# Optimization experiments

Hardware: AMD Instinct MI355X
Metric: run time of the kernel (lower is better)

Reference implementation:

```python
import jax, jax.numpy as jnp
import numpy as np

B, N, C = 16, 8192, 64
NPOINT, NSAMPLE = 1024, 32
RADIUS = 0.1


def setup_inputs() -> dict:
    key = jax.random.key(0)
    ks = jax.random.split(key, 6)
    xyz = jax.random.uniform(ks[0], (B, N, 3), jnp.float32)          # points in unit cube
    features = jax.random.normal(ks[1], (B, C, N), jnp.float32)
    W1 = jax.random.normal(ks[2], (64, 67), jnp.float32) * 0.1
    b1 = jnp.zeros((64,), jnp.float32)
    W2 = jax.random.normal(ks[3], (64, 64), jnp.float32) * 0.1
    b2 = jnp.zeros((64,), jnp.float32)
    W3 = jax.random.normal(ks[4], (128, 64), jnp.float32) * 0.1
    b3 = jnp.zeros((128,), jnp.float32)
    return dict(xyz=xyz, features=features, W1=W1, b1=b1, W2=W2, b2=b2, W3=W3, b3=b3)


def _fps(pts, npoint):
    """Furthest point sampling on a single cloud pts:(N,3) -> (npoint,) int32 indices."""
    n = pts.shape[0]
    def step(carry, _):
        dist, far = carry
        d = jnp.sum((pts - pts[far]) ** 2, axis=-1)   # (N,)
        dist = jnp.minimum(dist, d)
        return (dist, jnp.argmax(dist).astype(jnp.int32)), far
    init = (jnp.full((n,), 1e10, pts.dtype), jnp.int32(0))
    _, idx = jax.lax.scan(step, init, None, length=npoint)
    return idx


def reference(xyz, features, W1, b1, W2, b2, W3, b3):
    n = xyz.shape[1]
    # --- furthest point sample + gather centroids ---
    idx = jax.lax.stop_gradient(jax.vmap(lambda p: _fps(p, NPOINT))(xyz))   # (B,npoint)
    new_xyz = jnp.take_along_axis(xyz, idx[:, :, None], axis=1)             # (B,npoint,3)
    # --- ball query: first NSAMPLE indices with dist < r, pad with first hit (0 if none) ---
    d2 = jnp.sum((new_xyz[:, :, None, :] - xyz[:, None, :, :]) ** 2, axis=-1)  # (B,npoint,N)
    cand = jnp.where(d2 < RADIUS ** 2, jnp.arange(n, dtype=jnp.int32), n)
    sm = -jax.lax.top_k(-cand, NSAMPLE)[0]                                   # smallest NSAMPLE, ascending
    first = sm[..., :1]
    first = jnp.where(first == n, 0, first)
    gidx = jax.lax.stop_gradient(jnp.where(sm == n, first, sm))              # (B,npoint,nsample)
    # --- group: relative xyz + gathered features, concat on channel dim ---
    gxyz = jax.vmap(lambda p, i: p[i])(xyz, gidx)                            # (B,npoint,nsample,3)
    gxyz = (gxyz - new_xyz[:, :, None, :]).transpose(0, 3, 1, 2)             # (B,3,npoint,nsample)
    gfeat = jax.vmap(lambda f, i: f[:, i])(features, gidx)                   # (B,C,npoint,nsample)
    h = jnp.concatenate([gxyz, gfeat], axis=1)                               # (B,3+C,npoint,nsample)
    # --- shared MLP (1x1 conv + ReLU per layer) ---
    for W, b in ((W1, b1), (W2, b2), (W3, b3)):
        h = jax.nn.relu(jnp.einsum('oc,bcps->bops', W, h) + b[None, :, None, None])
    # --- max-pool over neighbors ---
    new_features = jnp.max(h, axis=-1)                                       # (B,128,npoint)
    return new_xyz, new_features
```

## Files before the change

### kernel.cpp

```cpp
#include <hip/hip_runtime.h>

#define BATCH   16
#define NPTS    8192
#define NCH     64
#define NPOINT  1024
#define NSAMPLE 32
#define R2      0.01f

#define DPP_RED_STAGE(CTRL)                                                   \
    {                                                                         \
        int lo = (int)(unsigned)(key & 0xffffffffull);                        \
        int hi = (int)(unsigned)(key >> 32);                                  \
        int mlo = __builtin_amdgcn_update_dpp(lo, lo, CTRL, 0xF, 0xF, false); \
        int mhi = __builtin_amdgcn_update_dpp(hi, hi, CTRL, 0xF, 0xF, false); \
        unsigned long long mk =                                               \
            ((unsigned long long)(unsigned)mhi << 32) | (unsigned)mlo;        \
        if (mk > key) key = mk;                                               \
    }

struct FpsShared {
    float pts[NPTS * 3];
    unsigned long long red[2][4];
    float ring_f[2][16][3];
};

__global__ __launch_bounds__(256, 1) void fps_tr_kernel(const float* __restrict__ xyz,
                                                        float* __restrict__ new_xyz,
                                                        const float* __restrict__ feat,
                                                        float* __restrict__ feat_t) {
    __shared__ union { FpsShared fps; float tile[64][65]; } U;
    const int t = threadIdx.x;

    if (blockIdx.x >= BATCH) {
        const int bidx = blockIdx.x - BATCH;
        const int b  = bidx >> 7;
        const int n0 = (bidx & 127) << 6;
        const int i  = t & 63, c0 = t >> 6;
        const float* src = feat + (size_t)b * NCH * NPTS;
#pragma unroll
        for (int r = 0; r < 16; ++r) {
            int c = c0 + r * 4;
            U.tile[c][i] = src[(size_t)c * NPTS + n0 + i];
        }
        __syncthreads();
        const int cc = t & 63, i0 = t >> 6;
        float* dst = feat_t + ((size_t)b * NPTS + n0) * NCH;
#pragma unroll
        for (int r = 0; r < 16; ++r) {
            int ii = i0 + r * 4;
            dst[(size_t)ii * NCH + cc] = U.tile[cc][ii];
        }
        return;
    }

    const int b = blockIdx.x;
    const float* g = xyz + (size_t)b * NPTS * 3;
    for (int i = t; i < NPTS * 3; i += 256) U.fps.pts[i] = g[i];
    __syncthreads();

    float px[32], py[32], pz[32], dist[32];
#pragma unroll
    for (int k = 0; k < 32; ++k) {
        const int p = t + (k << 8);
        px[k] = U.fps.pts[3 * p + 0];
        py[k] = U.fps.pts[3 * p + 1];
        pz[k] = U.fps.pts[3 * p + 2];
        dist[k] = 1e10f;
    }

    float fx = U.fps.pts[0], fy = U.fps.pts[1], fz = U.fps.pts[2];
    const int wave = t >> 6;

    for (int it = 0; it < NPOINT; ++it) {
        const int rb = (it >> 4) & 1, sl = it & 15;
        if (t == 0) {
            U.fps.ring_f[rb][sl][0] = fx;
            U.fps.ring_f[rb][sl][1] = fy;
            U.fps.ring_f[rb][sl][2] = fz;
        }
        float bestv = -1.0f; int bestk = 0;
#pragma unroll
        for (int k = 0; k < 32; ++k) {
            float dx = __fsub_rn(px[k], fx);
            float dy = __fsub_rn(py[k], fy);
            float dz = __fsub_rn(pz[k], fz);
            float d  = __fadd_rn(__fadd_rn(__fmul_rn(dx, dx), __fmul_rn(dy, dy)),
                                 __fmul_rn(dz, dz));
            float nd = fminf(dist[k], d);
            dist[k] = nd;
            if (nd > bestv) { bestv = nd; bestk = k; }
        }
        const int besti = t + (bestk << 8);
        unsigned long long key =
            ((unsigned long long)__float_as_uint(bestv) << 32) | (unsigned)(~besti);
        DPP_RED_STAGE(0x111)
        DPP_RED_STAGE(0x112)
        DPP_RED_STAGE(0x114)
        DPP_RED_STAGE(0x118)
        DPP_RED_STAGE(0x142)
        DPP_RED_STAGE(0x143)
        const int par = it & 1;
        if ((t & 63) == 63) U.fps.red[par][wave] = key;
        __syncthreads();

        if ((it & 15) == 15 && t < 48) {
            const int base0 = b * NPOINT + (it & ~15);
            new_xyz[(size_t)(base0 + t / 3) * 3 + (t % 3)] =
                U.fps.ring_f[rb][t / 3][t % 3];
        }

        unsigned long long kk = U.fps.red[par][0];
        unsigned long long k1 = U.fps.red[par][1];
        unsigned long long k2 = U.fps.red[par][2];
        unsigned long long k3 = U.fps.red[par][3];
        if (k1 > kk) kk = k1;
        if (k2 > kk) kk = k2;
        if (k3 > kk) kk = k3;
        const int far = (int)(~(unsigned)kk);
        fx = U.fps.pts[3 * far + 0];
        fy = U.fps.pts[3 * far + 1];
        fz = U.fps.pts[3 * far + 2];
    }
}

struct BqShared {
    float w1[64 * 68];
    float w2[64 * 64];
    float w3[128 * 64];
    float b1s[64], b2s[64], b3s[128];
    float cxyz[8][3];
    int   gidx[8][NSAMPLE];
};

__global__ __launch_bounds__(256) void bq_mlp_kernel(const float* __restrict__ xyz,
                                                     const float* __restrict__ feat_t,
                                                     const float* __restrict__ new_xyz,
                                                     const float* __restrict__ W1,
                                                     const float* __restrict__ b1,
                                                     const float* __restrict__ W2,
                                                     const float* __restrict__ b2,
                                                     const float* __restrict__ W3,
                                                     const float* __restrict__ b3,
                                                     float* __restrict__ out_feat) {
    __shared__ BqShared S;
    const int t = threadIdx.x;
    const int b  = blockIdx.x >> 7;
    const int p0 = (blockIdx.x & 127) << 3;

    for (int i = t; i < 64 * 67; i += 256) S.w1[(i / 67) * 68 + (i % 67)] = W1[i];
    if (t < 64) { S.w1[t * 68 + 67] = 0.0f; S.b1s[t] = b1[t]; S.b2s[t] = b2[t]; }
    if (t < 128) S.b3s[t] = b3[t];
    for (int i = t; i < 64 * 64; i += 256) S.w2[i] = W2[i];
    for (int i = t; i < 128 * 64; i += 256) S.w3[i] = W3[i];
    if (t < 24)
        S.cxyz[t / 3][t % 3] = new_xyz[((size_t)b * NPOINT + p0 + t / 3) * 3 + (t % 3)];
    __syncthreads();

    const int wv = t >> 6, lane = t & 63;
    const float* pts = xyz + (size_t)b * NPTS * 3;
    for (int q = 0; q < 2; ++q) {
        const int ci = wv * 2 + q;
        const float cx = S.cxyz[ci][0];
        const float cy = S.cxyz[ci][1];
        const float cz = S.cxyz[ci][2];
        int hits = 0, first = 0;
        for (int j0 = 0; j0 < NPTS; j0 += 64) {
            const int j = j0 + lane;
            float x = pts[3 * j], y = pts[3 * j + 1], z = pts[3 * j + 2];
            float dx = __fsub_rn(x, cx), dy = __fsub_rn(y, cy), dz = __fsub_rn(z, cz);
            float d2 = __fadd_rn(__fadd_rn(__fmul_rn(dx, dx), __fmul_rn(dy, dy)),
                                 __fmul_rn(dz, dz));
            const bool pred = d2 < R2;
            const unsigned long long mask = __ballot(pred);
            if (hits == 0 && mask)
                first = j0 + (int)(__ffsll((unsigned long long)mask) - 1);
            if (pred) {
                int slot = hits + (int)__popcll(mask & ((1ull << lane) - 1ull));
                if (slot < NSAMPLE) S.gidx[ci][slot] = j;
            }
            hits += (int)__popcll(mask);
            if (hits >= NSAMPLE) break;
        }
        if (hits < NSAMPLE && lane >= hits && lane < NSAMPLE)
            S.gidx[ci][lane] = first;
    }
    __syncthreads();

    const int ci = t >> 5, s = t & 31;
    const int p  = p0 + ci;
    const int gi = S.gidx[ci][s];
    const float nx0 = S.cxyz[ci][0];
    const float nx1 = S.cxyz[ci][1];
    const float nx2 = S.cxyz[ci][2];
    const float* pp = xyz + ((size_t)b * NPTS + gi) * 3;
    float h[68];
    h[0] = pp[0] - nx0;
    h[1] = pp[1] - nx1;
    h[2] = pp[2] - nx2;
    const float4* fp = (const float4*)(feat_t + ((size_t)b * NPTS + gi) * NCH);
#pragma unroll
    for (int qq = 0; qq < 16; ++qq) {
        float4 v = fp[qq];
        h[3 + 4 * qq] = v.x; h[4 + 4 * qq] = v.y;
        h[5 + 4 * qq] = v.z; h[6 + 4 * qq] = v.w;
    }
    h[67] = 0.0f;

    float h1[64];
#pragma unroll
    for (int o = 0; o < 64; ++o) {
        const float4* wr = (const float4*)(&S.w1[o * 68]);
        float a0 = 0.f, a1 = 0.f, a2 = 0.f, a3 = 0.f;
#pragma unroll
        for (int qq = 0; qq < 17; ++qq) {
            float4 w = wr[qq];
            a0 = fmaf(w.x, h[4 * qq + 0], a0);
            a1 = fmaf(w.y, h[4 * qq + 1], a1);
            a2 = fmaf(w.z, h[4 * qq + 2], a2);
            a3 = fmaf(w.w, h[4 * qq + 3], a3);
        }
        h1[o] = fmaxf((a0 + a1) + (a2 + a3) + S.b1s[o], 0.0f);
    }

    float h2[64];
#pragma unroll
    for (int o = 0; o < 64; ++o) {
        const float4* wr = (const float4*)(&S.w2[o * 64]);
        float a0 = 0.f, a1 = 0.f, a2 = 0.f, a3 = 0.f;
#pragma unroll
        for (int qq = 0; qq < 16; ++qq) {
            float4 w = wr[qq];
            a0 = fmaf(w.x, h1[4 * qq + 0], a0);
            a1 = fmaf(w.y, h1[4 * qq + 1], a1);
            a2 = fmaf(w.z, h1[4 * qq + 2], a2);
            a3 = fmaf(w.w, h1[4 * qq + 3], a3);
        }
        h2[o] = fmaxf((a0 + a1) + (a2 + a3) + S.b2s[o], 0.0f);
    }

    float* outp = out_feat + ((size_t)b * 128) * NPOINT + p;
#pragma unroll
    for (int o = 0; o < 128; ++o) {
        const float4* wr = (const float4*)(&S.w3[o * 64]);
        float a0 = 0.f, a1 = 0.f, a2 = 0.f, a3 = 0.f;
#pragma unroll
        for (int qq = 0; qq < 16; ++qq) {
            float4 w = wr[qq];
            a0 = fmaf(w.x, h2[4 * qq + 0], a0);
            a1 = fmaf(w.y, h2[4 * qq + 1], a1);
            a2 = fmaf(w.z, h2[4 * qq + 2], a2);
            a3 = fmaf(w.w, h2[4 * qq + 3], a3);
        }
        float acc = fmaxf((a0 + a1) + (a2 + a3) + S.b3s[o], 0.0f);
#pragma unroll
        for (int m = 1; m < 32; m <<= 1) acc = fmaxf(acc, __shfl_xor(acc, m, 64));
        if (s == 0) outp[(size_t)o * NPOINT] = acc;
    }
}

extern "C" void kernel_launch(void* const* d_in, const int* in_sizes, int n_in,
                              void* d_out, int out_size, void* d_ws, size_t ws_size,
                              hipStream_t stream) {
    const float* xyz  = (const float*)d_in[0];
    const float* feat = (const float*)d_in[1];
    const float* W1   = (const float*)d_in[2];
    const float* b1   = (const float*)d_in[3];
    const float* W2   = (const float*)d_in[4];
    const float* b2   = (const float*)d_in[5];
    const float* W3   = (const float*)d_in[6];
    const float* b3   = (const float*)d_in[7];

    float* new_xyz  = (float*)d_out;
    float* out_feat = (float*)d_out + (size_t)BATCH * NPOINT * 3;

    float* feat_t = (float*)d_ws;

    hipLaunchKernelGGL(fps_tr_kernel, dim3(BATCH + BATCH * (NPTS / 64)), dim3(256), 0,
                       stream, xyz, new_xyz, feat, feat_t);
    hipLaunchKernelGGL(bq_mlp_kernel, dim3(BATCH * NPOINT / 8), dim3(256), 0, stream,
                       xyz, feat_t, new_xyz,
                       W1, b1, W2, b2, W3, b3, out_feat);
}
```

Measured before the change: 1.948 ms.

## Widen FPS to 512 threads and restage MLP as shared-memory register-tiled GEMM

FPS blocks now use 512 threads, with 16 points per thread and an 8-way cross-wave reduction, to shorten the serial per-iteration scan. The bq_mlp kernel handles 4 centroids per block. Grouped features are staged in shared memory and each layer runs as a register-tiled outer-product GEMM over transposed weights, replacing per-thread 68-wide register vectors. The aim is to cut the register pressure and repeated weight reads of the old per-sample matvec. In exchange it adds large LDS use (about 120KB, limiting occupancy to one block per CU), extra barriers, and shuffle reductions for the max-pool.

```diff
diff --git a/kernel.cpp b/kernel.cpp
--- a/kernel.cpp
+++ b/kernel.cpp
@@ -20,11 +20,11 @@
 
 struct FpsShared {
     float pts[NPTS * 3];
-    unsigned long long red[2][4];
+    unsigned long long red[2][8];
     float ring_f[2][16][3];
 };
 
-__global__ __launch_bounds__(256, 1) void fps_tr_kernel(const float* __restrict__ xyz,
+__global__ __launch_bounds__(512, 1) void fps_tr_kernel(const float* __restrict__ xyz,
                                                         float* __restrict__ new_xyz,
                                                         const float* __restrict__ feat,
                                                         float* __restrict__ feat_t) {
@@ -38,16 +38,16 @@
         const int i  = t & 63, c0 = t >> 6;
         const float* src = feat + (size_t)b * NCH * NPTS;
 #pragma unroll
-        for (int r = 0; r < 16; ++r) {
-            int c = c0 + r * 4;
+        for (int r = 0; r < 8; ++r) {
+            int c = c0 + r * 8;
             U.tile[c][i] = src[(size_t)c * NPTS + n0 + i];
         }
         __syncthreads();
         const int cc = t & 63, i0 = t >> 6;
         float* dst = feat_t + ((size_t)b * NPTS + n0) * NCH;
 #pragma unroll
-        for (int r = 0; r < 16; ++r) {
-            int ii = i0 + r * 4;
+        for (int r = 0; r < 8; ++r) {
+            int ii = i0 + r * 8;
             dst[(size_t)ii * NCH + cc] = U.tile[cc][ii];
         }
         return;
@@ -55,13 +55,13 @@
 
     const int b = blockIdx.x;
     const float* g = xyz + (size_t)b * NPTS * 3;
-    for (int i = t; i < NPTS * 3; i += 256) U.fps.pts[i] = g[i];
-    __syncthreads();
-
-    float px[32], py[32], pz[32], dist[32];
-#pragma unroll
-    for (int k = 0; k < 32; ++k) {
-        const int p = t + (k << 8);
+    for (int i = t; i < NPTS * 3; i += 512) U.fps.pts[i] = g[i];
+    __syncthreads();
+
+    float px[16], py[16], pz[16], dist[16];
+#pragma unroll
+    for (int k = 0; k < 16; ++k) {
+        const int p = t + (k << 9);
         px[k] = U.fps.pts[3 * p + 0];
         py[k] = U.fps.pts[3 * p + 1];
         pz[k] = U.fps.pts[3 * p + 2];
@@ -80,7 +80,7 @@
         }
         float bestv = -1.0f; int bestk = 0;
 #pragma unroll
-        for (int k = 0; k < 32; ++k) {
+        for (int k = 0; k < 16; ++k) {
             float dx = __fsub_rn(px[k], fx);
             float dy = __fsub_rn(py[k], fy);
             float dz = __fsub_rn(pz[k], fz);
@@ -90,7 +90,7 @@
             dist[k] = nd;
             if (nd > bestv) { bestv = nd; bestk = k; }
         }
-        const int besti = t + (bestk << 8);
+        const int besti = t + (bestk << 9);
         unsigned long long key =
             ((unsigned long long)__float_as_uint(bestv) << 32) | (unsigned)(~besti);
         DPP_RED_STAGE(0x111)
@@ -110,12 +110,11 @@
         }
 
         unsigned long long kk = U.fps.red[par][0];
-        unsigned long long k1 = U.fps.red[par][1];
-        unsigned long long k2 = U.fps.red[par][2];
-        unsigned long long k3 = U.fps.red[par][3];
-        if (k1 > kk) kk = k1;
-        if (k2 > kk) kk = k2;
-        if (k3 > kk) kk = k3;
+#pragma unroll
+        for (int e = 1; e < 8; ++e) {
+            unsigned long long ke = U.fps.red[par][e];
+            if (ke > kk) kk = ke;
+        }
         const int far = (int)(~(unsigned)kk);
         fx = U.fps.pts[3 * far + 0];
         fy = U.fps.pts[3 * far + 1];
@@ -123,49 +122,60 @@
     }
 }
 
-struct BqShared {
-    float w1[64 * 68];
-    float w2[64 * 64];
-    float w3[128 * 64];
+struct MlpShared {
+    float w1t[67 * 68];
+    float w2t[64 * 68];
+    float w3t[64 * 132];
+    float h0[128 * 67];
+    float h1[128 * 67];
     float b1s[64], b2s[64], b3s[128];
-    float cxyz[8][3];
-    int   gidx[8][NSAMPLE];
+    float cxyz[4][3];
+    int   gidx[4][NSAMPLE];
 };
 
-__global__ __launch_bounds__(256) void bq_mlp_kernel(const float* __restrict__ xyz,
-                                                     const float* __restrict__ feat_t,
-                                                     const float* __restrict__ new_xyz,
-                                                     const float* __restrict__ W1,
-                                                     const float* __restrict__ b1,
-                                                     const float* __restrict__ W2,
-                                                     const float* __restrict__ b2,
-                                                     const float* __restrict__ W3,
-                                                     const float* __restrict__ b3,
-                                                     float* __restrict__ out_feat) {
-    __shared__ BqShared S;
+__global__ __launch_bounds__(256, 1) void bq_mlp_kernel(const float* __restrict__ xyz,
+                                                        const float* __restrict__ feat_t,
+                                                        const float* __restrict__ new_xyz,
+                                                        const float* __restrict__ W1,
+                                                        const float* __restrict__ b1,
+                                                        const float* __restrict__ W2,
+                                                        const float* __restrict__ b2,
+                                                        const float* __restrict__ W3,
+                                                        const float* __restrict__ b3,
+                                                        float* __restrict__ out_feat) {
+    __shared__ MlpShared S;
     const int t = threadIdx.x;
-    const int b  = blockIdx.x >> 7;
-    const int p0 = (blockIdx.x & 127) << 3;
-
-    for (int i = t; i < 64 * 67; i += 256) S.w1[(i / 67) * 68 + (i % 67)] = W1[i];
-    if (t < 64) { S.w1[t * 68 + 67] = 0.0f; S.b1s[t] = b1[t]; S.b2s[t] = b2[t]; }
+    const int b  = blockIdx.x >> 8;
+    const int p0 = (blockIdx.x & 255) << 2;
+
+    for (int i = t; i < 67 * 64; i += 256) {
+        const int o = i / 67, kk = i % 67;
+        const int ks = (kk < 3) ? (64 + kk) : (kk - 3);
+        S.w1t[ks * 68 + o] = W1[i];
+    }
+    for (int i = t; i < 64 * 64; i += 256) {
+        const int o = i >> 6, k = i & 63;
+        S.w2t[k * 68 + o] = W2[i];
+    }
+    for (int i = t; i < 128 * 64; i += 256) {
+        const int o = i >> 6, k = i & 63;
+        S.w3t[k * 132 + o] = W3[i];
+    }
+    if (t < 64)  { S.b1s[t] = b1[t]; S.b2s[t] = b2[t]; }
     if (t < 128) S.b3s[t] = b3[t];
-    for (int i = t; i < 64 * 64; i += 256) S.w2[i] = W2[i];
-    for (int i = t; i < 128 * 64; i += 256) S.w3[i] = W3[i];
-    if (t < 24)
+    if (t < 12)
         S.cxyz[t / 3][t % 3] = new_xyz[((size_t)b * NPOINT + p0 + t / 3) * 3 + (t % 3)];
     __syncthreads();
 
-    const int wv = t >> 6, lane = t & 63;
-    const float* pts = xyz + (size_t)b * NPTS * 3;
-    for (int q = 0; q < 2; ++q) {
-        const int ci = wv * 2 + q;
-        const float cx = S.cxyz[ci][0];
-        const float cy = S.cxyz[ci][1];
-        const float cz = S.cxyz[ci][2];
+    const int wv = t >> 6, l = t & 63;
+    {
+        const float* pts = xyz + (size_t)b * NPTS * 3;
+        const float cx = S.cxyz[wv][0];
+        const float cy = S.cxyz[wv][1];
+        const float cz = S.cxyz[wv][2];
         int hits = 0, first = 0;
         for (int j0 = 0; j0 < NPTS; j0 += 64) {
-            const int j = j0 + lane;
+            const int j = j0 + l;
             float x = pts[3 * j], y = pts[3 * j + 1], z = pts[3 * j + 2];
             float dx = __fsub_rn(x, cx), dy = __fsub_rn(y, cy), dz = __fsub_rn(z, cz);
             float d2 = __fadd_rn(__fadd_rn(__fmul_rn(dx, dx), __fmul_rn(dy, dy)),
@@ -175,86 +185,150 @@
             if (hits == 0 && mask)
                 first = j0 + (int)(__ffsll((unsigned long long)mask) - 1);
             if (pred) {
-                int slot = hits + (int)__popcll(mask & ((1ull << lane) - 1ull));
-                if (slot < NSAMPLE) S.gidx[ci][slot] = j;
+                int slot = hits + (int)__popcll(mask & ((1ull << l) - 1ull));
+                if (slot < NSAMPLE) S.gidx[wv][slot] = j;
             }
             hits += (int)__popcll(mask);
             if (hits >= NSAMPLE) break;
         }
-        if (hits < NSAMPLE && lane >= hits && lane < NSAMPLE)
-            S.gidx[ci][lane] = first;
-    }
-    __syncthreads();
-
-    const int ci = t >> 5, s = t & 31;
-    const int p  = p0 + ci;
-    const int gi = S.gidx[ci][s];
-    const float nx0 = S.cxyz[ci][0];
-    const float nx1 = S.cxyz[ci][1];
-    const float nx2 = S.cxyz[ci][2];
-    const float* pp = xyz + ((size_t)b * NPTS + gi) * 3;
-    float h[68];
-    h[0] = pp[0] - nx0;
-    h[1] = pp[1] - nx1;
-    h[2] = pp[2] - nx2;
-    const float4* fp = (const float4*)(feat_t + ((size_t)b * NPTS + gi) * NCH);
-#pragma unroll
-    for (int qq = 0; qq < 16; ++qq) {
-        float4 v = fp[qq];
-        h[3 + 4 * qq] = v.x; h[4 + 4 * qq] = v.y;
-        h[5 + 4 * qq] = v.z; h[6 + 4 * qq] = v.w;
-    }
-    h[67] = 0.0f;
-
-    float h1[64];
-#pragma unroll
-    for (int o = 0; o < 64; ++o) {
-        const float4* wr = (const float4*)(&S.w1[o * 68]);
-        float a0 = 0.f, a1 = 0.f, a2 = 0.f, a3 = 0.f;
-#pragma unroll
-        for (int qq = 0; qq < 17; ++qq) {
-            float4 w = wr[qq];
-            a0 = fmaf(w.x, h[4 * qq + 0], a0);
-            a1 = fmaf(w.y, h[4 * qq + 1], a1);
-            a2 = fmaf(w.z, h[4 * qq + 2], a2);
-            a3 = fmaf(w.w, h[4 * qq + 3], a3);
-        }
-        h1[o] = fmaxf((a0 + a1) + (a2 + a3) + S.b1s[o], 0.0f);
-    }
-
-    float h2[64];
-#pragma unroll
-    for (int o = 0; o < 64; ++o) {
-        const float4* wr = (const float4*)(&S.w2[o * 64]);
-        float a0 = 0.f, a1 = 0.f, a2 = 0.f, a3 = 0.f;
-#pragma unroll
-        for (int qq = 0; qq < 16; ++qq) {
-            float4 w = wr[qq];
-            a0 = fmaf(w.x, h1[4 * qq + 0], a0);
-            a1 = fmaf(w.y, h1[4 * qq + 1], a1);
-            a2 = fmaf(w.z, h1[4 * qq + 2], a2);
-            a3 = fmaf(w.w, h1[4 * qq + 3], a3);
-        }
-        h2[o] = fmaxf((a0 + a1) + (a2 + a3) + S.b2s[o], 0.0f);
-    }
-
-    float* outp = out_feat + ((size_t)b * 128) * NPOINT + p;
-#pragma unroll
-    for (int o = 0; o < 128; ++o) {
-        const float4* wr = (const float4*)(&S.w3[o * 64]);
-        float a0 = 0.f, a1 = 0.f, a2 = 0.f, a3 = 0.f;
-#pragma unroll
-        for (int qq = 0; qq < 16; ++qq) {
-            float4 w = wr[qq];
-            a0 = fmaf(w.x, h2[4 * qq + 0], a0);
-            a1 = fmaf(w.y, h2[4 * qq + 1], a1);
-            a2 = fmaf(w.z, h2[4 * qq + 2], a2);
-            a3 = fmaf(w.w, h2[4 * qq + 3], a3);
-        }
-        float acc = fmaxf((a0 + a1) + (a2 + a3) + S.b3s[o], 0.0f);
-#pragma unroll
-        for (int m = 1; m < 32; m <<= 1) acc = fmaxf(acc, __shfl_xor(acc, m, 64));
-        if (s == 0) outp[(size_t)o * NPOINT] = acc;
+        if (hits < NSAMPLE && l >= hits && l < NSAMPLE)
+            S.gidx[wv][l] = first;
+    }
+    __syncthreads();
+
+    {
+        const int c = t >> 1, half = t & 1;
+        const int ci = c >> 5, s = c & 31;
+        const int gi = S.gidx[ci][s];
+        float* hr = &S.h0[c * 67];
+        const float4* fp = (const float4*)(feat_t + ((size_t)b * NPTS + gi) * NCH);
+        const int q0 = half * 8;
+#pragma unroll
+        for (int q = 0; q < 8; ++q) {
+            float4 v = fp[q0 + q];
+            hr[4 * (q0 + q) + 0] = v.x;
+            hr[4 * (q0 + q) + 1] = v.y;
+            hr[4 * (q0 + q) + 2] = v.z;
+            hr[4 * (q0 + q) + 3] = v.w;
+        }
+        if (half == 1) {
+            const float* pp = xyz + ((size_t)b * NPTS + gi) * 3;
+            hr[64] = pp[0] - S.cxyz[ci][0];
+            hr[65] = pp[1] - S.cxyz[ci][1];
+            hr[66] = pp[2] - S.cxyz[ci][2];
+        }
+    }
+    __syncthreads();
+
+    {
+        const float* h0r0 = &S.h0[l * 67];
+        const float* h0r1 = &S.h0[(l + 64) * 67];
+        const int o0 = wv << 4;
+        float a[16][2];
+#pragma unroll
+        for (int oo = 0; oo < 16; ++oo) { a[oo][0] = 0.f; a[oo][1] = 0.f; }
+        for (int k = 0; k < 67; ++k) {
+            const float hc0 = h0r0[k], hc1 = h0r1[k];
+            const float4* wr = (const float4*)(&S.w1t[k * 68 + o0]);
+#pragma unroll
+            for (int m = 0; m < 4; ++m) {
+                float4 w = wr[m];
+                a[4*m+0][0] = fmaf(w.x, hc0, a[4*m+0][0]);
+                a[4*m+0][1] = fmaf(w.x, hc1, a[4*m+0][1]);
+                a[4*m+1][0] = fmaf(w.y, hc0, a[4*m+1][0]);
+                a[4*m+1][1] = fmaf(w.y, hc1, a[4*m+1][1]);
+                a[4*m+2][0] = fmaf(w.z, hc0, a[4*m+2][0]);
+                a[4*m+2][1] = fmaf(w.z, hc1, a[4*m+2][1]);
+                a[4*m+3][0] = fmaf(w.w, hc0, a[4*m+3][0]);
+                a[4*m+3][1] = fmaf(w.w, hc1, a[4*m+3][1]);
+            }
+        }
+#pragma unroll
+        for (int oo = 0; oo < 16; ++oo) {
+            const int o = o0 + oo;
+            const float bb = S.b1s[o];
+            S.h1[l * 67 + o]        = fmaxf(a[oo][0] + bb, 0.f);
+            S.h1[(l + 64) * 67 + o] = fmaxf(a[oo][1] + bb, 0.f);
+        }
+    }
+    __syncthreads();
+
+    {
+        const float* h1r0 = &S.h1[l * 67];
+        const float* h1r1 = &S.h1[(l + 64) * 67];
+        const int o0 = wv << 4;
+        float a[16][2];
+#pragma unroll
+        for (int oo = 0; oo < 16; ++oo) { a[oo][0] = 0.f; a[oo][1] = 0.f; }
+        for (int k = 0; k < 64; ++k) {
+            const float hc0 = h1r0[k], hc1 = h1r1[k];
+            const float4* wr = (const float4*)(&S.w2t[k * 68 + o0]);
+#pragma unroll
+            for (int m = 0; m < 4; ++m) {
+                float4 w = wr[m];
+                a[4*m+0][0] = fmaf(w.x, hc0, a[4*m+0][0]);
+                a[4*m+0][1] = fmaf(w.x, hc1, a[4*m+0][1]);
+                a[4*m+1][0] = fmaf(w.y, hc0, a[4*m+1][0]);
+                a[4*m+1][1] = fmaf(w.y, hc1, a[4*m+1][1]);
+                a[4*m+2][0] = fmaf(w.z, hc0, a[4*m+2][0]);
+                a[4*m+2][1] = fmaf(w.z, hc1, a[4*m+2][1]);
+                a[4*m+3][0] = fmaf(w.w, hc0, a[4*m+3][0]);
+                a[4*m+3][1] = fmaf(w.w, hc1, a[4*m+3][1]);
+            }
+        }
+#pragma unroll
+        for (int oo = 0; oo < 16; ++oo) {
+            const int o = o0 + oo;
+            const float bb = S.b2s[o];
+            S.h0[l * 67 + o]        = fmaxf(a[oo][0] + bb, 0.f);
+            S.h0[(l + 64) * 67 + o] = fmaxf(a[oo][1] + bb, 0.f);
+        }
+    }
+    __syncthreads();
+
+    {
+        const float* h2r0 = &S.h0[l * 67];
+        const float* h2r1 = &S.h0[(l + 64) * 67];
+        const int o0 = wv << 5;
+        float a[32][2];
+#pragma unroll
+        for (int oo = 0; oo < 32; ++oo) { a[oo][0] = 0.f; a[oo][1] = 0.f; }
+        for (int k = 0; k < 64; ++k) {
+            const float hc0 = h2r0[k], hc1 = h2r1[k];
+            const float4* wr = (const float4*)(&S.w3t[k * 132 + o0]);
+#pragma unroll
+            for (int m = 0; m < 8; ++m) {
+                float4 w = wr[m];
+                a[4*m+0][0] = fmaf(w.x, hc0, a[4*m+0][0]);
+                a[4*m+0][1] = fmaf(w.x, hc1, a[4*m+0][1]);
+                a[4*m+1][0] = fmaf(w.y, hc0, a[4*m+1][0]);
+                a[4*m+1][1] = fmaf(w.y, hc1, a[4*m+1][1]);
+                a[4*m+2][0] = fmaf(w.z, hc0, a[4*m+2][0]);
+                a[4*m+2][1] = fmaf(w.z, hc1, a[4*m+2][1]);
+                a[4*m+3][0] = fmaf(w.w, hc0, a[4*m+3][0]);
+                a[4*m+3][1] = fmaf(w.w, hc1, a[4*m+3][1]);
+            }
+        }
+        const int s = l & 31;
+        float out0 = 0.f, out1 = 0.f;
+#pragma unroll
+        for (int oo = 0; oo < 32; ++oo) {
+            const float bb = S.b3s[o0 + oo];
+            float r0 = fmaxf(a[oo][0] + bb, 0.f);
+            float r1 = fmaxf(a[oo][1] + bb, 0.f);
+#pragma unroll
+            for (int m = 1; m < 32; m <<= 1) {
+                r0 = fmaxf(r0, __shfl_xor(r0, m, 64));
+                r1 = fmaxf(r1, __shfl_xor(r1, m, 64));
+            }
+            if (s == oo) { out0 = r0; out1 = r1; }
+        }
+        const int o   = o0 + s;
+        const int ci0 = l >> 5;
+        const int ci1 = 2 + (l >> 5);
+        float* outp = out_feat + ((size_t)b * 128 + o) * NPOINT + p0;
+        outp[ci0] = out0;
+        outp[ci1] = out1;
     }
 }
 
@@ -275,9 +349,9 @@
 
     float* feat_t = (float*)d_ws;
 
-    hipLaunchKernelGGL(fps_tr_kernel, dim3(BATCH + BATCH * (NPTS / 64)), dim3(256), 0,
+    hipLaunchKernelGGL(fps_tr_kernel, dim3(BATCH + BATCH * (NPTS / 64)), dim3(512), 0,
                        stream, xyz, new_xyz, feat, feat_t);
-    hipLaunchKernelGGL(bq_mlp_kernel, dim3(BATCH * NPOINT / 8), dim3(256), 0, stream,
+    hipLaunchKernelGGL(bq_mlp_kernel, dim3(BATCH * NPOINT / 4), dim3(256), 0, stream,
                        xyz, feat_t, new_xyz,
                        W1, b1, W2, b2, W3, b3, out_feat);
 }
```

After: 2.135 ms. 9.6% more time.
